# Kernel optimization log

Hardware: AMD Instinct MI355X
Metric: run time of the kernel (lower is better)

## Reference

```python
import jax, jax.numpy as jnp
import numpy as np

B, L, D_MODEL = 4, 2048, 1024
N_HEADS, FEAT, HEAD_DIM = 16, 16, 64
CHUNK = 128
EPS = 1e-12


def taylor_exp(x):
    """2nd-order Taylor feature map of exp(q.k/sqrt(d)).
    x: (b, h, l, f) -> (b, h, l, 1 + f + f*f)"""
    f = x.shape[-1]
    r2 = jnp.sqrt(jnp.asarray(2.0, x.dtype))
    rd = jnp.sqrt(jnp.asarray(float(f), x.dtype))      # sqrt(d)
    rrd = jnp.sqrt(rd)                                  # d**0.25
    x2 = (x[..., :, None] * x[..., None, :]).reshape(*x.shape[:-1], f * f) / r2
    ones = jnp.ones_like(x[..., :1])
    return jnp.concatenate([ones, x / rrd, x2 / rd], axis=-1)


def setup_inputs() -> dict:
    key = jax.random.key(0)
    k1, k2, k3, k4, k5 = jax.random.split(key, 5)
    s = 0.02
    return {
        "hidden_states": jax.random.normal(k1, (B, L, D_MODEL), jnp.float32),
        "Wq": jax.random.normal(k2, (N_HEADS * FEAT, D_MODEL), jnp.float32) * s,
        "Wk": jax.random.normal(k3, (N_HEADS * FEAT, D_MODEL), jnp.float32) * s,
        "Wv": jax.random.normal(k4, (N_HEADS * HEAD_DIM, D_MODEL), jnp.float32) * s,
        "Wo": jax.random.normal(k5, (D_MODEL, N_HEADS * HEAD_DIM), jnp.float32) * s,
    }


def reference(hidden_states, Wq, Wk, Wv, Wo):
    b, l, _ = hidden_states.shape
    # projections (Linear without bias: x @ W.T)
    q = (hidden_states @ Wq.T).reshape(b, l, N_HEADS, FEAT).transpose(0, 2, 1, 3)
    k = (hidden_states @ Wk.T).reshape(b, l, N_HEADS, FEAT).transpose(0, 2, 1, 3)
    v = (hidden_states @ Wv.T).reshape(b, l, N_HEADS, HEAD_DIM).transpose(0, 2, 1, 3)

    qf = taylor_exp(q)  # (b, h, l, De) with De = 1 + f + f^2 = 273
    kf = taylor_exp(k)
    De = qf.shape[-1]

    # chunked causal linear attention: same math as cumulative kv-state
    n = l // CHUNK
    qc = jnp.moveaxis(qf.reshape(b, N_HEADS, n, CHUNK, De), 2, 0)       # (n,b,h,c,De)
    kc = jnp.moveaxis(kf.reshape(b, N_HEADS, n, CHUNK, De), 2, 0)
    vc = jnp.moveaxis(v.reshape(b, N_HEADS, n, CHUNK, HEAD_DIM), 2, 0)
    mask = jnp.tril(jnp.ones((CHUNK, CHUNK), qf.dtype))

    def step(carry, xs):
        S, z = carry                       # S: (b,h,De,e), z: (b,h,De)
        qi, ki, vi = xs
        attn = jnp.einsum('bhid,bhjd->bhij', qi, ki) * mask
        num = jnp.einsum('bhij,bhje->bhie', attn, vi) \
            + jnp.einsum('bhid,bhde->bhie', qi, S)
        den = attn.sum(-1) + jnp.einsum('bhid,bhd->bhi', qi, z)
        yi = num / (den[..., None] + EPS)
        S = S + jnp.einsum('bhjd,bhje->bhde', ki, vi)
        z = z + ki.sum(2)
        return (S, z), yi

    S0 = jnp.zeros((b, N_HEADS, De, HEAD_DIM), qf.dtype)
    z0 = jnp.zeros((b, N_HEADS, De), qf.dtype)
    _, ys = jax.lax.scan(step, (S0, z0), (qc, kc, vc))
    y = jnp.moveaxis(ys, 0, 2).reshape(b, N_HEADS, l, HEAD_DIM)          # (b,h,l,e)
    y = y.transpose(0, 2, 1, 3).reshape(b, l, N_HEADS * HEAD_DIM)        # (b,l,h*e)
    return y @ Wo.T
```

## Files before the change

kernel.cpp:

```cpp
#include <hip/hip_runtime.h>
#include <hip/hip_bf16.h>

#define BB 4
#define LL 2048
#define DM 1024
#define NH 16
#define FEAT 16
#define HD 64
#define CHUNK 128
#define NCHUNK 16
#define NEXT 80
#define SROW 23040
#define EPS 1e-12f
#define INV_R2RD 0.17677669529663688f
#define QKVLD 1536

typedef short bf16x8_t __attribute__((ext_vector_type(8)));
typedef float f32x4_t  __attribute__((ext_vector_type(4)));

__device__ __forceinline__ float b2f(unsigned short u) {
    union { unsigned int i; float f; } x; x.i = ((unsigned int)u) << 16; return x.f;
}
__device__ __forceinline__ unsigned short f2b(float f) {
    __hip_bfloat16 h = __float2bfloat16(f);
    return *reinterpret_cast<unsigned short*>(&h);
}

__global__ __launch_bounds__(256)
void cast_all(const float* __restrict__ hs, const float* __restrict__ wq,
              const float* __restrict__ wk, const float* __restrict__ wv,
              const float* __restrict__ wo, unsigned short* __restrict__ hs_bf,
              unsigned short* __restrict__ wqkv, unsigned short* __restrict__ wo_bf)
{
    const int i = (blockIdx.x * 256 + threadIdx.x) * 4;
    const float* s; unsigned short* d;
    if (i < 8388608)       { s = hs + i;             d = hs_bf + i; }
    else if (i < 8650752)  { s = wq + (i - 8388608); d = wqkv + (i - 8388608); }
    else if (i < 8912896)  { s = wk + (i - 8650752); d = wqkv + 262144 + (i - 8650752); }
    else if (i < 9961472)  { s = wv + (i - 8912896); d = wqkv + 524288 + (i - 8912896); }
    else if (i < 11010048) { s = wo + (i - 9961472); d = wo_bf + (i - 9961472); }
    else return;
    float4 v = *(const float4*)s;
    ushort4 o; o.x = f2b(v.x); o.y = f2b(v.y); o.z = f2b(v.z); o.w = f2b(v.w);
    *(ushort4*)d = o;
}

template <typename OutT>
__global__ __launch_bounds__(512, 2)
void gemm_bf16_8ph(const unsigned short* __restrict__ A, const unsigned short* __restrict__ Bw,
                   OutT* __restrict__ C, int K, int lda, int ldb, int ldc)
{
    __shared__ unsigned short lds[65536];
    const int tid  = threadIdx.x;
    const int wid  = tid >> 6, lane = tid & 63;
    const int wm   = wid >> 2, wn = wid & 3;
    const int ml   = lane & 15, quad = lane >> 4;
    const int nwg = gridDim.x * gridDim.y;
    const int lin = blockIdx.y * gridDim.x + blockIdx.x;
    const int swz_id = (lin & 7) * (nwg >> 3) + (lin >> 3);
    const int m0   = (swz_id / gridDim.x) * 256, n0 = (swz_id % gridDim.x) * 256;
    const int NT   = K >> 6;

    const int srow  = tid >> 3;
    const int scol  = ((tid & 7) ^ (srow & 7)) << 3;
    const int wbase = wid << 9;

    auto stage_half = [&](int t, int isB, int h) {
        const unsigned short* g0 = isB ? Bw : A;
        const int ld = isB ? ldb : lda;
        const int rb = (isB ? n0 : m0) + h * 128 + srow;
        const int k0 = t << 6;
        unsigned short* lb = lds + (isB ? 32768 : 0) + ((t & 1) << 14) + (h << 13) + wbase;
#pragma unroll
        for (int l = 0; l < 2; ++l) {
            const unsigned short* g = g0 + (size_t)(rb + l * 64) * ld + k0 + scol;
            __builtin_amdgcn_global_load_lds((const __attribute__((address_space(1))) void*)g,
                                             (__attribute__((address_space(3))) void*)(lb + l * 4096),
                                             16, 0, 0);
        }
    };

    f32x4_t acc[8][4];
#pragma unroll
    for (int i = 0; i < 8; ++i)
#pragma unroll
        for (int j = 0; j < 4; ++j) acc[i][j] = (f32x4_t){0.f, 0.f, 0.f, 0.f};

    stage_half(0, 0, 0); stage_half(0, 1, 0); stage_half(0, 0, 1); stage_half(0, 1, 1);
    stage_half(1, 0, 0); stage_half(1, 1, 0); stage_half(1, 0, 1);
    asm volatile("s_waitcnt vmcnt(6)" ::: "memory");
    __builtin_amdgcn_s_barrier();

    const int swz  = (ml & 7) << 3;
    const int c0   = (quad << 3) ^ swz;
    const int c1   = (32 + (quad << 3)) ^ swz;
    const int arow = ml << 6;

    bf16x8_t aA[4][2], bLo[2][2], bHi[2][2];

    for (int t = 0; t < NT; ++t) {
        const int ab = (t & 1) << 14;
        const int bb = 32768 + ((t & 1) << 14);

#pragma unroll
        for (int m = 0; m < 4; ++m) {
            const int r = ab + ((2 * m + wm) << 10) + arow;
            aA[m][0] = *(const bf16x8_t*)&lds[r + c0];
            aA[m][1] = *(const bf16x8_t*)&lds[r + c1];
        }
#pragma unroll
        for (int n = 0; n < 2; ++n) {
            const int r = bb + ((4 * n + wn) << 10) + arow;
            bLo[n][0] = *(const bf16x8_t*)&lds[r + c0];
            bLo[n][1] = *(const bf16x8_t*)&lds[r + c1];
        }
        if (t + 1 < NT) stage_half(t + 1, 1, 1);
        __builtin_amdgcn_s_barrier();
        asm volatile("s_waitcnt lgkmcnt(0)" ::: "memory");
        __builtin_amdgcn_sched_barrier(0);
        __builtin_amdgcn_s_setprio(1);
#pragma unroll
        for (int m = 0; m < 4; ++m)
#pragma unroll
            for (int n = 0; n < 2; ++n) {
                acc[m][n] = __builtin_amdgcn_mfma_f32_16x16x32_bf16(aA[m][0], bLo[n][0], acc[m][n], 0, 0, 0);
                acc[m][n] = __builtin_amdgcn_mfma_f32_16x16x32_bf16(aA[m][1], bLo[n][1], acc[m][n], 0, 0, 0);
            }
        __builtin_amdgcn_s_setprio(0);
        __builtin_amdgcn_s_barrier();

#pragma unroll
        for (int n = 0; n < 2; ++n) {
            const int r = bb + ((4 * (n + 2) + wn) << 10) + arow;
            bHi[n][0] = *(const bf16x8_t*)&lds[r + c0];
            bHi[n][1] = *(const bf16x8_t*)&lds[r + c1];
        }
        if (t + 2 < NT) stage_half(t + 2, 0, 0);
        __builtin_amdgcn_s_barrier();
        asm volatile("s_waitcnt lgkmcnt(0)" ::: "memory");
        __builtin_amdgcn_sched_barrier(0);
        __builtin_amdgcn_s_setprio(1);
#pragma unroll
        for (int m = 0; m < 4; ++m)
#pragma unroll
            for (int n = 0; n < 2; ++n) {
                acc[m][2 + n] = __builtin_amdgcn_mfma_f32_16x16x32_bf16(aA[m][0], bHi[n][0], acc[m][2 + n], 0, 0, 0);
                acc[m][2 + n] = __builtin_amdgcn_mfma_f32_16x16x32_bf16(aA[m][1], bHi[n][1], acc[m][2 + n], 0, 0, 0);
            }
        __builtin_amdgcn_s_setprio(0);
        __builtin_amdgcn_s_barrier();

#pragma unroll
        for (int m = 0; m < 4; ++m) {
            const int r = ab + ((2 * (m + 4) + wm) << 10) + arow;
            aA[m][0] = *(const bf16x8_t*)&lds[r + c0];
            aA[m][1] = *(const bf16x8_t*)&lds[r + c1];
        }
        if (t + 2 < NT) stage_half(t + 2, 1, 0);
        __builtin_amdgcn_s_barrier();
        asm volatile("s_waitcnt lgkmcnt(0)" ::: "memory");
        __builtin_amdgcn_sched_barrier(0);
        __builtin_amdgcn_s_setprio(1);
#pragma unroll
        for (int m = 0; m < 4; ++m)
#pragma unroll
            for (int n = 0; n < 2; ++n) {
                acc[4 + m][2 + n] = __builtin_amdgcn_mfma_f32_16x16x32_bf16(aA[m][0], bHi[n][0], acc[4 + m][2 + n], 0, 0, 0);
                acc[4 + m][2 + n] = __builtin_amdgcn_mfma_f32_16x16x32_bf16(aA[m][1], bHi[n][1], acc[4 + m][2 + n], 0, 0, 0);
            }
        __builtin_amdgcn_s_setprio(0);
        __builtin_amdgcn_s_barrier();

        if (t + 2 < NT) stage_half(t + 2, 0, 1);
        __builtin_amdgcn_s_barrier();
        asm volatile("s_waitcnt lgkmcnt(0)" ::: "memory");
        __builtin_amdgcn_sched_barrier(0);
        __builtin_amdgcn_s_setprio(1);
#pragma unroll
        for (int m = 0; m < 4; ++m)
#pragma unroll
            for (int n = 0; n < 2; ++n) {
                acc[4 + m][n] = __builtin_amdgcn_mfma_f32_16x16x32_bf16(aA[m][0], bLo[n][0], acc[4 + m][n], 0, 0, 0);
                acc[4 + m][n] = __builtin_amdgcn_mfma_f32_16x16x32_bf16(aA[m][1], bLo[n][1], acc[4 + m][n], 0, 0, 0);
            }
        __builtin_amdgcn_s_setprio(0);
        if (t + 2 < NT)      asm volatile("s_waitcnt vmcnt(6)" ::: "memory");
        else if (t + 1 < NT) asm volatile("s_waitcnt vmcnt(0)" ::: "memory");
        __builtin_amdgcn_s_barrier();
    }

#pragma unroll
    for (int m = 0; m < 8; ++m) {
        const int rbase = m0 + (2 * m + wm) * 16 + quad * 4;
#pragma unroll
        for (int n = 0; n < 4; ++n) {
            const int col = n0 + (4 * n + wn) * 16 + ml;
#pragma unroll
            for (int r = 0; r < 4; ++r) {
                const float v = acc[m][n][r];
                if constexpr (sizeof(OutT) == 2) {
                    ((unsigned short*)C)[(size_t)(rbase + r) * ldc + col] = f2b(v);
                } else {
                    ((float*)C)[(size_t)(rbase + r) * ldc + col] = v;
                }
            }
        }
    }
}

__global__ __launch_bounds__(512, 2)
void gemm_bf16_128x256(const unsigned short* __restrict__ A, const unsigned short* __restrict__ Bw,
                       float* __restrict__ C, int K, int lda, int ldb, int ldc)
{
    __shared__ unsigned short lds[49152];
    const int tid  = threadIdx.x;
    const int wid  = tid >> 6, lane = tid & 63;
    const int wm   = wid >> 2, wn = wid & 3;
    const int ml   = lane & 15, quad = lane >> 4;
    const int nwg = gridDim.x * gridDim.y;
    const int lin = blockIdx.y * gridDim.x + blockIdx.x;
    const int swz_id = (lin & 7) * (nwg >> 3) + (lin >> 3);
    const int m0   = (swz_id / gridDim.x) * 128, n0 = (swz_id % gridDim.x) * 256;
    const int NT   = K >> 6;

    const int srow  = tid >> 3;
    const int scol  = ((tid & 7) ^ (srow & 7)) << 3;
    const int wbase = wid << 9;

    auto stage_unit = [&](int t, int isB, int u) {
        const unsigned short* g0 = isB ? Bw : A;
        const int ld = isB ? ldb : lda;
        const int rb = (isB ? n0 : m0) + u * 64 + srow;
        const int k0 = t << 6;
        unsigned short* lb = lds + (isB ? 16384 : 0) + ((t & 1) << (isB ? 14 : 13))
                             + (u << 12) + wbase;
        const unsigned short* g = g0 + (size_t)rb * ld + k0 + scol;
        __builtin_amdgcn_global_load_lds((const __attribute__((address_space(1))) void*)g,
                                         (__attribute__((address_space(3))) void*)lb, 16, 0, 0);
    };

    f32x4_t acc[4][4];
#pragma unroll
    for (int i = 0; i < 4; ++i)
#pragma unroll
        for (int j = 0; j < 4; ++j) acc[i][j] = (f32x4_t){0.f, 0.f, 0.f, 0.f};

    stage_unit(0, 0, 0); stage_unit(0, 0, 1);
    stage_unit(0, 1, 0); stage_unit(0, 1, 1); stage_unit(0, 1, 2); stage_unit(0, 1, 3);
    stage_unit(1, 0, 0); stage_unit(1, 0, 1);
    stage_unit(1, 1, 0); stage_unit(1, 1, 1);
    asm volatile("s_waitcnt vmcnt(4)" ::: "memory");
    __builtin_amdgcn_s_barrier();

    const int swz  = (ml & 7) << 3;
    const int c0   = (quad << 3) ^ swz;
    const int c1   = (32 + (quad << 3)) ^ swz;
    const int arow = ml << 6;

    bf16x8_t aA[4][2], bF[2][2];

    for (int t = 0; t < NT; ++t) {
        const int ab = (t & 1) << 13;
        const int bb = 16384 + ((t & 1) << 14);

#pragma unroll
        for (int m = 0; m < 4; ++m) {
            const int r = ab + ((2 * m + wm) << 10) + arow;
            aA[m][0] = *(const bf16x8_t*)&lds[r + c0];
            aA[m][1] = *(const bf16x8_t*)&lds[r + c1];
        }
#pragma unroll
        for (int n = 0; n < 2; ++n) {
            const int r = bb + ((4 * n + wn) << 10) + arow;
            bF[n][0] = *(const bf16x8_t*)&lds[r + c0];
            bF[n][1] = *(const bf16x8_t*)&lds[r + c1];
        }
        if (t + 1 < NT) { stage_unit(t + 1, 1, 2); stage_unit(t + 1, 1, 3); }
        __builtin_amdgcn_s_barrier();
        asm volatile("s_waitcnt lgkmcnt(0)" ::: "memory");
        __builtin_amdgcn_sched_barrier(0);
        __builtin_amdgcn_s_setprio(1);
#pragma unroll
        for (int m = 0; m < 4; ++m)
#pragma unroll
            for (int n = 0; n < 2; ++n) {
                acc[m][n] = __builtin_amdgcn_mfma_f32_16x16x32_bf16(aA[m][0], bF[n][0], acc[m][n], 0, 0, 0);
                acc[m][n] = __builtin_amdgcn_mfma_f32_16x16x32_bf16(aA[m][1], bF[n][1], acc[m][n], 0, 0, 0);
            }
        __builtin_amdgcn_s_setprio(0);
        __builtin_amdgcn_s_barrier();

#pragma unroll
        for (int n = 0; n < 2; ++n) {
            const int r = bb + ((4 * (n + 2) + wn) << 10) + arow;
            bF[n][0] = *(const bf16x8_t*)&lds[r + c0];
            bF[n][1] = *(const bf16x8_t*)&lds[r + c1];
        }
        if (t + 2 < NT) {
            stage_unit(t + 2, 0, 0); stage_unit(t + 2, 0, 1);
            stage_unit(t + 2, 1, 0); stage_unit(t + 2, 1, 1);
        }
        __builtin_amdgcn_s_barrier();
        asm volatile("s_waitcnt lgkmcnt(0)" ::: "memory");
        __builtin_amdgcn_sched_barrier(0);
        __builtin_amdgcn_s_setprio(1);
#pragma unroll
        for (int m = 0; m < 4; ++m)
#pragma unroll
            for (int n = 0; n < 2; ++n) {
                acc[m][2 + n] = __builtin_amdgcn_mfma_f32_16x16x32_bf16(aA[m][0], bF[n][0], acc[m][2 + n], 0, 0, 0);
                acc[m][2 + n] = __builtin_amdgcn_mfma_f32_16x16x32_bf16(aA[m][1], bF[n][1], acc[m][2 + n], 0, 0, 0);
            }
        __builtin_amdgcn_s_setprio(0);
        if (t + 2 < NT)      asm volatile("s_waitcnt vmcnt(4)" ::: "memory");
        else if (t + 1 < NT) asm volatile("s_waitcnt vmcnt(0)" ::: "memory");
        __builtin_amdgcn_s_barrier();
    }

#pragma unroll
    for (int m = 0; m < 4; ++m) {
        const int rbase = m0 + (2 * m + wm) * 16 + quad * 4;
#pragma unroll
        for (int n = 0; n < 4; ++n) {
            const int col = n0 + (4 * n + wn) * 16 + ml;
#pragma unroll
            for (int r = 0; r < 4; ++r)
                C[(size_t)(rbase + r) * ldc + col] = acc[m][n][r];
        }
    }
}

__global__ __launch_bounds__(256)
void state_kernel(const unsigned short* __restrict__ qkv, unsigned short* __restrict__ STg)
{
    __shared__ unsigned short KT[16 * 136];
    __shared__ unsigned short VT[80 * 136];

    const int x = blockIdx.x;
    const int c = x & 15, bh = x >> 4;
    const int b = bh >> 4, h = bh & 15;
    const int tid = threadIdx.x;
    const int wave = tid >> 6, lane = tid & 63;
    const int ml = lane & 15, kg8 = (lane >> 4) * 8;
    const size_t rowbase = (size_t)(b * LL + c * CHUNK);
    const size_t Sbase = (size_t)x * SROW;

    {
        const int row = tid >> 1, half = tid & 1;
        uint4 kv = *(const uint4*)(qkv + (rowbase + row) * QKVLD + 256 + h * 16 + half * 8);
        const unsigned short* kp = (const unsigned short*)&kv;
#pragma unroll
        for (int i = 0; i < 8; ++i) KT[(half * 8 + i) * 136 + row] = kp[i];
#pragma unroll
        for (int cc = 0; cc < 4; ++cc) {
            uint4 vv = *(const uint4*)(qkv + (rowbase + row) * QKVLD + 512 + h * 64 + half * 32 + cc * 8);
            const unsigned short* vp = (const unsigned short*)&vv;
#pragma unroll
            for (int i = 0; i < 8; ++i) VT[(half * 32 + cc * 8 + i) * 136 + row] = vp[i];
        }
        if (half == 0) {
            VT[64 * 136 + row] = 0x3F80;
        } else {
#pragma unroll
            for (int e = 65; e < 80; ++e) VT[e * 136 + row] = 0;
        }
    }
    __syncthreads();

    bf16x8_t bfr[5][4];
#pragma unroll
    for (int nt = 0; nt < 5; ++nt)
#pragma unroll
        for (int ks = 0; ks < 4; ++ks)
            bfr[nt][ks] = *(const bf16x8_t*)&VT[(nt * 16 + ml) * 136 + ks * 32 + kg8];

    for (int mt = wave; mt < 18; mt += 4) {
        const int d = mt * 16 + ml;
        bf16x8_t af[4];
#pragma unroll
        for (int ks = 0; ks < 4; ++ks) {
            const int jb = ks * 32 + kg8;
            unsigned short o[8];
            if (d >= 24 && d < 280) {
                const int e = d - 24, a = e >> 4, bq = e & 15;
                bf16x8_t ka = *(const bf16x8_t*)&KT[a  * 136 + jb];
                bf16x8_t kb = *(const bf16x8_t*)&KT[bq * 136 + jb];
#pragma unroll
                for (int j = 0; j < 8; ++j)
                    o[j] = f2b(b2f((unsigned short)ka[j]) * b2f((unsigned short)kb[j]) * INV_R2RD);
            } else if (d == 0) {
#pragma unroll
                for (int j = 0; j < 8; ++j) o[j] = 0x3F80;
            } else if (d <= 16) {
                bf16x8_t kx = *(const bf16x8_t*)&KT[(d - 1) * 136 + jb];
#pragma unroll
                for (int j = 0; j < 8; ++j) o[j] = f2b(b2f((unsigned short)kx[j]) * 0.5f);
            } else {
#pragma unroll
                for (int j = 0; j < 8; ++j) o[j] = 0;
            }
            af[ks] = *(const bf16x8_t*)o;
        }
        f32x4_t acc[5];
#pragma unroll
        for (int nt = 0; nt < 5; ++nt) acc[nt] = (f32x4_t){0.f, 0.f, 0.f, 0.f};
        __builtin_amdgcn_s_setprio(1);
#pragma unroll
        for (int nt = 0; nt < 5; ++nt)
#pragma unroll
            for (int ks = 0; ks < 4; ++ks)
                acc[nt] = __builtin_amdgcn_mfma_f32_16x16x32_bf16(af[ks], bfr[nt][ks], acc[nt], 0, 0, 0);
        __builtin_amdgcn_s_setprio(0);
#pragma unroll
        for (int nt = 0; nt < 5; ++nt) {
            ushort4 pk;
            pk.x = f2b(acc[nt][0]); pk.y = f2b(acc[nt][1]);
            pk.z = f2b(acc[nt][2]); pk.w = f2b(acc[nt][3]);
            *(ushort4*)(STg + Sbase + (size_t)mt * 1280 + (nt * 16 + ml) * 16 + (lane >> 4) * 4) = pk;
        }
    }
}

__global__ __launch_bounds__(256)
void scan_S(unsigned short* __restrict__ STg) {
    const int bh  = blockIdx.y;
    const int idx = blockIdx.x * 256 + threadIdx.x;
    if (idx >= SROW / 8) return;
    const size_t base = (size_t)bh * NCHUNK * SROW + (size_t)idx * 8;
    uint4 v[NCHUNK];
#pragma unroll
    for (int c = 0; c < NCHUNK; ++c)
        v[c] = *(const uint4*)(STg + base + (size_t)c * SROW);
    float acc[8] = {};
#pragma unroll
    for (int c = 0; c < NCHUNK; ++c) {
        const unsigned short* vp = (const unsigned short*)&v[c];
        uint4 o;
        unsigned short* op = (unsigned short*)&o;
#pragma unroll
        for (int i = 0; i < 8; ++i) { op[i] = f2b(acc[i]); acc[i] += b2f(vp[i]); }
        *(uint4*)(STg + base + (size_t)c * SROW) = o;
    }
}

#define OFF_VT 0
#define OFF_QP 0
#define OFF_KP 5120
#define OFF_A  10880
#define OFF_QS 28288

__global__ __launch_bounds__(256)
void out_kernel(const unsigned short* __restrict__ qkv_ro, const unsigned short* __restrict__ STg,
                unsigned short* __restrict__ qkv_w)
{
    __shared__ unsigned short smem[30336];

    const int x = blockIdx.x;
    const int c = x & 15, bh = x >> 4;
    const int b = bh >> 4, h = bh & 15;
    const int tid = threadIdx.x;
    const int w = tid >> 6, lane = tid & 63;
    const int ml = lane & 15, quad = lane >> 4, kg8 = quad * 8;
    const size_t rowbase = (size_t)(b * LL + c * CHUNK);
    const size_t Sbase = (size_t)x * SROW;

    const unsigned short* stp = STg + Sbase + (size_t)(quad >> 1) * 1280 + (quad & 1) * 8;
    bf16x8_t stf[2][5];
#pragma unroll
    for (int nt = 0; nt < 5; ++nt)
        stf[0][nt] = *(const bf16x8_t*)(stp + (nt * 16 + ml) * 16);

    {
        const int row = tid >> 1, half = tid & 1;
        uint4 qv = *(const uint4*)(qkv_ro + (rowbase + row) * QKVLD + h * 16 + half * 8);
        *(uint4*)&smem[OFF_QP + row * 40 + half * 8] = qv;
        *(uint4*)&smem[OFF_QP + row * 40 + 16 + half * 8] = (uint4){0, 0, 0, 0};
        *(uint4*)&smem[OFF_QS + row * 16 + half * 8] = qv;
        uint4 kv = *(const uint4*)(qkv_ro + (rowbase + row) * QKVLD + 256 + h * 16 + half * 8);
        *(uint4*)&smem[OFF_KP + row * 40 + half * 8] = kv;
        *(uint4*)&smem[OFF_KP + row * 40 + 16 + half * 8] = (uint4){0, 0, 0, 0};
    }
    __syncthreads();

    {
        bf16x8_t q0 = *(const bf16x8_t*)&smem[OFF_QP + (w * 32 + ml) * 40 + kg8];
        bf16x8_t q1 = *(const bf16x8_t*)&smem[OFF_QP + (w * 32 + 16 + ml) * 40 + kg8];
#pragma unroll
        for (int nt = 0; nt < 8; ++nt) {
            bf16x8_t kf = *(const bf16x8_t*)&smem[OFF_KP + (nt * 16 + ml) * 40 + kg8];
            f32x4_t a0 = __builtin_amdgcn_mfma_f32_16x16x32_bf16(q0, kf, (f32x4_t){0,0,0,0}, 0, 0, 0);
            f32x4_t a1 = __builtin_amdgcn_mfma_f32_16x16x32_bf16(q1, kf, (f32x4_t){0,0,0,0}, 0, 0, 0);
            const int j = nt * 16 + ml;
#pragma unroll
            for (int r = 0; r < 4; ++r) {
                int i0 = w * 32 + quad * 4 + r;
                float s0 = a0[r] * 0.25f;
                float v0 = (j <= i0) ? (1.f + s0 + 0.5f * s0 * s0) : 0.f;
                smem[OFF_A + i0 * 136 + j] = f2b(v0);
                int i1 = i0 + 16;
                float s1 = a1[r] * 0.25f;
                float v1 = (j <= i1) ? (1.f + s1 + 0.5f * s1 * s1) : 0.f;
                smem[OFF_A + i1 * 136 + j] = f2b(v1);
            }
        }
    }
    const int r0 = w * 32 + ml, r1 = r0 + 16;
    float qA[16], qB[16];
    {
        bf16x8_t t0 = *(const bf16x8_t*)&smem[OFF_QS + r0 * 16];
        bf16x8_t t1 = *(const bf16x8_t*)&smem[OFF_QS + r0 * 16 + 8];
        bf16x8_t t2 = *(const bf16x8_t*)&smem[OFF_QS + r1 * 16];
        bf16x8_t t3 = *(const bf16x8_t*)&smem[OFF_QS + r1 * 16 + 8];
#pragma unroll
        for (int i = 0; i < 8; ++i) {
            qA[i] = b2f((unsigned short)t0[i]); qA[8 + i] = b2f((unsigned short)t1[i]);
            qB[i] = b2f((unsigned short)t2[i]); qB[8 + i] = b2f((unsigned short)t3[i]);
        }
    }
    __syncthreads();

    {
        const int row = tid >> 1, half = tid & 1;
#pragma unroll
        for (int cc = 0; cc < 4; ++cc) {
            uint4 vv = *(const uint4*)(qkv_ro + (rowbase + row) * QKVLD + 512 + h * 64 + half * 32 + cc * 8);
            const unsigned short* vp = (const unsigned short*)&vv;
#pragma unroll
            for (int i = 0; i < 8; ++i) smem[OFF_VT + (half * 32 + cc * 8 + i) * 136 + row] = vp[i];
        }
        if (half == 0) {
            smem[OFF_VT + 64 * 136 + row] = 0x3F80;
        } else {
#pragma unroll
            for (int e = 65; e < 80; ++e) smem[OFF_VT + e * 136 + row] = 0;
        }
    }
    __syncthreads();

    f32x4_t acc[2][5];
#pragma unroll
    for (int mt = 0; mt < 2; ++mt)
#pragma unroll
        for (int nt = 0; nt < 5; ++nt) acc[mt][nt] = (f32x4_t){0.f, 0.f, 0.f, 0.f};

#pragma unroll
    for (int ks = 0; ks < 4; ++ks) {
        bf16x8_t af0 = *(const bf16x8_t*)&smem[OFF_A + (w * 32 + ml) * 136 + ks * 32 + kg8];
        bf16x8_t af1 = *(const bf16x8_t*)&smem[OFF_A + (w * 32 + 16 + ml) * 136 + ks * 32 + kg8];
        __builtin_amdgcn_s_setprio(1);
#pragma unroll
        for (int nt = 0; nt < 5; ++nt) {
            bf16x8_t bv = *(const bf16x8_t*)&smem[OFF_VT + (nt * 16 + ml) * 136 + ks * 32 + kg8];
            acc[0][nt] = __builtin_amdgcn_mfma_f32_16x16x32_bf16(af0, bv, acc[0][nt], 0, 0, 0);
            acc[1][nt] = __builtin_amdgcn_mfma_f32_16x16x32_bf16(af1, bv, acc[1][nt], 0, 0, 0);
        }
        __builtin_amdgcn_s_setprio(0);
    }

#pragma unroll
    for (int kq = 0; kq < 9; ++kq) {
        if (kq < 8) {
#pragma unroll
            for (int nt = 0; nt < 5; ++nt)
                stf[(kq + 1) & 1][nt] =
                    *(const bf16x8_t*)(stp + (size_t)(kq + 1) * 2560 + (nt * 16 + ml) * 16);
        }
        bf16x8_t qf[2];
#pragma unroll
        for (int mt = 0; mt < 2; ++mt) {
            const float* q = (mt == 0) ? qA : qB;
            const int qsrow = (mt == 0) ? r0 : r1;
            const int d0 = kq * 32 + kg8;
            unsigned short o[8];
            if (d0 >= 24 && d0 < 280) {
                const int e0 = d0 - 24;
                const float qa = b2f(smem[OFF_QS + qsrow * 16 + (e0 >> 4)]) * INV_R2RD;
                if ((e0 & 15) == 0) {
#pragma unroll
                    for (int j = 0; j < 8; ++j) o[j] = f2b(qa * q[j]);
                } else {
#pragma unroll
                    for (int j = 0; j < 8; ++j) o[j] = f2b(qa * q[8 + j]);
                }
            } else if (d0 == 0) {
                o[0] = 0x3F80;
#pragma unroll
                for (int j = 1; j < 8; ++j) o[j] = f2b(q[j - 1] * 0.5f);
            } else if (d0 == 8) {
#pragma unroll
                for (int j = 0; j < 8; ++j) o[j] = f2b(q[7 + j] * 0.5f);
            } else if (d0 == 16) {
                o[0] = f2b(q[15] * 0.5f);
#pragma unroll
                for (int j = 1; j < 8; ++j) o[j] = 0;
            } else {
#pragma unroll
                for (int j = 0; j < 8; ++j) o[j] = 0;
            }
            qf[mt] = *(const bf16x8_t*)o;
        }
        __builtin_amdgcn_s_setprio(1);
#pragma unroll
        for (int nt = 0; nt < 5; ++nt) {
            acc[0][nt] = __builtin_amdgcn_mfma_f32_16x16x32_bf16(qf[0], stf[kq & 1][nt], acc[0][nt], 0, 0, 0);
            acc[1][nt] = __builtin_amdgcn_mfma_f32_16x16x32_bf16(qf[1], stf[kq & 1][nt], acc[1][nt], 0, 0, 0);
        }
        __builtin_amdgcn_s_setprio(0);
    }

#pragma unroll
    for (int mt = 0; mt < 2; ++mt) {
        float den[4];
#pragma unroll
        for (int r = 0; r < 4; ++r) den[r] = __shfl(acc[mt][4][r], lane & 48);
#pragma unroll
        for (int r = 0; r < 4; ++r) {
            const size_t grow = rowbase + w * 32 + mt * 16 + quad * 4 + r;
            const float rc = 1.f / (den[r] + EPS);
#pragma unroll
            for (int nt = 0; nt < 4; ++nt)
                qkv_w[grow * QKVLD + 512 + h * 64 + nt * 16 + ml] = f2b(acc[mt][nt][r] * rc);
        }
    }
}

extern "C" void kernel_launch(void* const* d_in, const int* in_sizes, int n_in,
                              void* d_out, int out_size, void* d_ws, size_t ws_size,
                              hipStream_t stream)
{
    (void)in_sizes; (void)n_in; (void)out_size; (void)ws_size;
    const float* hs = (const float*)d_in[0];
    const float* Wq = (const float*)d_in[1];
    const float* Wk = (const float*)d_in[2];
    const float* Wv = (const float*)d_in[3];
    const float* Wo = (const float*)d_in[4];
    float* out = (float*)d_out;

    char* ws = (char*)d_ws;
    unsigned short* STg   = (unsigned short*)ws;
    unsigned short* hs_bf = (unsigned short*)ws;
    size_t off = 47185920;
    unsigned short* qkv   = (unsigned short*)(ws + off); off += 25165824;
    unsigned short* Wqkv  = (unsigned short*)(ws + off); off += 3145728;
    unsigned short* Wo_bf = (unsigned short*)(ws + off); off += 2097152;

    cast_all<<<10752, 256, 0, stream>>>(hs, Wq, Wk, Wv, Wo, hs_bf, Wqkv, Wo_bf);
    gemm_bf16_8ph<unsigned short><<<dim3(6, 32), 512, 0, stream>>>(hs_bf, Wqkv, qkv,
                                                                   DM, DM, DM, QKVLD);
    state_kernel<<<1024, 256, 0, stream>>>(qkv, STg);
    scan_S<<<dim3(12, 64), 256, 0, stream>>>(STg);
    out_kernel<<<1024, 256, 0, stream>>>(qkv, STg, qkv);
    gemm_bf16_128x256<<<dim3(4, 64), 512, 0, stream>>>(qkv + 512, Wo_bf, out,
                                                       DM, QKVLD, DM, DM);
}
```

Before: 201.9 us.

## Compact per-chunk state layout and triple-buffer state loads in output kernel

```diff
diff --git a/kernel.cpp b/kernel.cpp
--- a/kernel.cpp
+++ b/kernel.cpp
@@ -9,8 +9,8 @@
 #define HD 64
 #define CHUNK 128
 #define NCHUNK 16
-#define NEXT 80
-#define SROW 23040
+#define NEXT 65
+#define SROW 18720
 #define EPS 1e-12f
 #define INV_R2RD 0.17677669529663688f
 #define QKVLD 1536
@@ -342,6 +342,7 @@
     const int tid = threadIdx.x;
     const int wave = tid >> 6, lane = tid & 63;
     const int ml = lane & 15, kg8 = (lane >> 4) * 8;
+    const int quad4 = (lane >> 4) * 4;
     const size_t rowbase = (size_t)(b * LL + c * CHUNK);
     const size_t Sbase = (size_t)x * SROW;
 
@@ -416,7 +417,11 @@
             ushort4 pk;
             pk.x = f2b(acc[nt][0]); pk.y = f2b(acc[nt][1]);
             pk.z = f2b(acc[nt][2]); pk.w = f2b(acc[nt][3]);
-            *(ushort4*)(STg + Sbase + (size_t)mt * 1280 + (nt * 16 + ml) * 16 + (lane >> 4) * 4) = pk;
+            if (nt < 4) {
+                *(ushort4*)(STg + Sbase + (size_t)mt * 1040 + (nt * 16 + ml) * 16 + quad4) = pk;
+            } else if (ml == 0) {
+                *(ushort4*)(STg + Sbase + (size_t)mt * 1040 + 1024 + quad4) = pk;
+            }
         }
     }
 }
@@ -447,13 +452,12 @@
 #define OFF_QP 0
 #define OFF_KP 5120
 #define OFF_A  10880
-#define OFF_QS 28288
 
 __global__ __launch_bounds__(256)
 void out_kernel(const unsigned short* __restrict__ qkv_ro, const unsigned short* __restrict__ STg,
                 unsigned short* __restrict__ qkv_w)
 {
-    __shared__ unsigned short smem[30336];
+    __shared__ unsigned short smem[28288];
 
     const int x = blockIdx.x;
     const int c = x & 15, bh = x >> 4;
@@ -464,22 +468,28 @@
     const size_t rowbase = (size_t)(b * LL + c * CHUNK);
     const size_t Sbase = (size_t)x * SROW;
 
-    const unsigned short* stp = STg + Sbase + (size_t)(quad >> 1) * 1280 + (quad & 1) * 8;
-    bf16x8_t stf[2][5];
-#pragma unroll
-    for (int nt = 0; nt < 5; ++nt)
-        stf[0][nt] = *(const bf16x8_t*)(stp + (nt * 16 + ml) * 16);
-
-    {
-        const int row = tid >> 1, half = tid & 1;
-        uint4 qv = *(const uint4*)(qkv_ro + (rowbase + row) * QKVLD + h * 16 + half * 8);
-        *(uint4*)&smem[OFF_QP + row * 40 + half * 8] = qv;
-        *(uint4*)&smem[OFF_QP + row * 40 + 16 + half * 8] = (uint4){0, 0, 0, 0};
-        *(uint4*)&smem[OFF_QS + row * 16 + half * 8] = qv;
-        uint4 kv = *(const uint4*)(qkv_ro + (rowbase + row) * QKVLD + 256 + h * 16 + half * 8);
-        *(uint4*)&smem[OFF_KP + row * 40 + half * 8] = kv;
-        *(uint4*)&smem[OFF_KP + row * 40 + 16 + half * 8] = (uint4){0, 0, 0, 0};
-    }
+    const unsigned short* stp = STg + Sbase + (size_t)(quad >> 1) * 1040 + (quad & 1) * 8;
+    bf16x8_t stf[3][5];
+    auto ldst = [&](int kq, int slot) {
+#pragma unroll
+        for (int nt = 0; nt < 5; ++nt)
+            stf[slot][nt] = *(const bf16x8_t*)(stp + (size_t)kq * 2080 + (nt * 16 + ml) * 16);
+    };
+
+    const int row = tid >> 1, half = tid & 1;
+    uint4 qv = *(const uint4*)(qkv_ro + (rowbase + row) * QKVLD + h * 16 + half * 8);
+    uint4 kv = *(const uint4*)(qkv_ro + (rowbase + row) * QKVLD + 256 + h * 16 + half * 8);
+    uint4 vreg[4];
+#pragma unroll
+    for (int cc = 0; cc < 4; ++cc)
+        vreg[cc] = *(const uint4*)(qkv_ro + (rowbase + row) * QKVLD + 512 + h * 64 + half * 32 + cc * 8);
+    ldst(0, 0);
+    ldst(1, 1);
+
+    *(uint4*)&smem[OFF_QP + row * 40 + half * 8] = qv;
+    *(uint4*)&smem[OFF_QP + row * 40 + 16 + half * 8] = (uint4){0, 0, 0, 0};
+    *(uint4*)&smem[OFF_KP + row * 40 + half * 8] = kv;
+    *(uint4*)&smem[OFF_KP + row * 40 + 16 + half * 8] = (uint4){0, 0, 0, 0};
     __syncthreads();
 
     {
@@ -507,24 +517,28 @@
     const int r0 = w * 32 + ml, r1 = r0 + 16;
     float qA[16], qB[16];
     {
-        bf16x8_t t0 = *(const bf16x8_t*)&smem[OFF_QS + r0 * 16];
-        bf16x8_t t1 = *(const bf16x8_t*)&smem[OFF_QS + r0 * 16 + 8];
-        bf16x8_t t2 = *(const bf16x8_t*)&smem[OFF_QS + r1 * 16];
-        bf16x8_t t3 = *(const bf16x8_t*)&smem[OFF_QS + r1 * 16 + 8];
+        bf16x8_t t0 = *(const bf16x8_t*)&smem[OFF_QP + r0 * 40];
+        bf16x8_t t1 = *(const bf16x8_t*)&smem[OFF_QP + r0 * 40 + 8];
+        bf16x8_t t2 = *(const bf16x8_t*)&smem[OFF_QP + r1 * 40];
+        bf16x8_t t3 = *(const bf16x8_t*)&smem[OFF_QP + r1 * 40 + 8];
 #pragma unroll
         for (int i = 0; i < 8; ++i) {
             qA[i] = b2f((unsigned short)t0[i]); qA[8 + i] = b2f((unsigned short)t1[i]);
             qB[i] = b2f((unsigned short)t2[i]); qB[8 + i] = b2f((unsigned short)t3[i]);
         }
     }
+    float qselA[8], qselB[8];
+#pragma unroll
+    for (int j = 0; j < 8; ++j) {
+        qselA[j] = (quad & 1) ? qA[j] : qA[8 + j];
+        qselB[j] = (quad & 1) ? qB[j] : qB[8 + j];
+    }
     __syncthreads();
 
     {
-        const int row = tid >> 1, half = tid & 1;
 #pragma unroll
         for (int cc = 0; cc < 4; ++cc) {
-            uint4 vv = *(const uint4*)(qkv_ro + (rowbase + row) * QKVLD + 512 + h * 64 + half * 32 + cc * 8);
-            const unsigned short* vp = (const unsigned short*)&vv;
+            const unsigned short* vp = (const unsigned short*)&vreg[cc];
 #pragma unroll
             for (int i = 0; i < 8; ++i) smem[OFF_VT + (half * 32 + cc * 8 + i) * 136 + row] = vp[i];
         }
@@ -542,6 +556,8 @@
     for (int mt = 0; mt < 2; ++mt)
 #pragma unroll
         for (int nt = 0; nt < 5; ++nt) acc[mt][nt] = (f32x4_t){0.f, 0.f, 0.f, 0.f};
+
+    ldst(2, 2);
 
 #pragma unroll
     for (int ks = 0; ks < 4; ++ks) {
@@ -559,29 +575,21 @@
 
 #pragma unroll
     for (int kq = 0; kq < 9; ++kq) {
-        if (kq < 8) {
-#pragma unroll
-            for (int nt = 0; nt < 5; ++nt)
-                stf[(kq + 1) & 1][nt] =
-                    *(const bf16x8_t*)(stp + (size_t)(kq + 1) * 2560 + (nt * 16 + ml) * 16);
-        }
         bf16x8_t qf[2];
 #pragma unroll
         for (int mt = 0; mt < 2; ++mt) {
-            const float* q = (mt == 0) ? qA : qB;
-            const int qsrow = (mt == 0) ? r0 : r1;
+            const float* q    = (mt == 0) ? qA : qB;
+            const float* qsel = (mt == 0) ? qselA : qselB;
             const int d0 = kq * 32 + kg8;
             unsigned short o[8];
             if (d0 >= 24 && d0 < 280) {
-                const int e0 = d0 - 24;
-                const float qa = b2f(smem[OFF_QS + qsrow * 16 + (e0 >> 4)]) * INV_R2RD;
-                if ((e0 & 15) == 0) {
-#pragma unroll
-                    for (int j = 0; j < 8; ++j) o[j] = f2b(qa * q[j]);
-                } else {
-#pragma unroll
-                    for (int j = 0; j < 8; ++j) o[j] = f2b(qa * q[8 + j]);
-                }
+                const int i2 = 2 * kq;
+                const float base = (quad == 3) ? q[i2 > 15 ? 15 : i2]
+                                 : (quad == 0) ? q[i2 < 2 ? 0 : i2 - 2]
+                                               : q[i2 < 1 ? 0 : i2 - 1];
+                const float qa = base * INV_R2RD;
+#pragma unroll
+                for (int j = 0; j < 8; ++j) o[j] = f2b(qa * qsel[j]);
             } else if (d0 == 0) {
                 o[0] = 0x3F80;
 #pragma unroll
@@ -602,10 +610,11 @@
         __builtin_amdgcn_s_setprio(1);
 #pragma unroll
         for (int nt = 0; nt < 5; ++nt) {
-            acc[0][nt] = __builtin_amdgcn_mfma_f32_16x16x32_bf16(qf[0], stf[kq & 1][nt], acc[0][nt], 0, 0, 0);
-            acc[1][nt] = __builtin_amdgcn_mfma_f32_16x16x32_bf16(qf[1], stf[kq & 1][nt], acc[1][nt], 0, 0, 0);
-        }
-        __builtin_amdgcn_s_setprio(0);
+            acc[0][nt] = __builtin_amdgcn_mfma_f32_16x16x32_bf16(qf[0], stf[kq % 3][nt], acc[0][nt], 0, 0, 0);
+            acc[1][nt] = __builtin_amdgcn_mfma_f32_16x16x32_bf16(qf[1], stf[kq % 3][nt], acc[1][nt], 0, 0, 0);
+        }
+        __builtin_amdgcn_s_setprio(0);
+        if (kq + 3 < 9) ldst(kq + 3, kq % 3);
     }
 
 #pragma unroll
@@ -648,7 +657,7 @@
     gemm_bf16_8ph<unsigned short><<<dim3(6, 32), 512, 0, stream>>>(hs_bf, Wqkv, qkv,
                                                                    DM, DM, DM, QKVLD);
     state_kernel<<<1024, 256, 0, stream>>>(qkv, STg);
-    scan_S<<<dim3(12, 64), 256, 0, stream>>>(STg);
+    scan_S<<<dim3(10, 64), 256, 0, stream>>>(STg);
     out_kernel<<<1024, 256, 0, stream>>>(qkv, STg, qkv);
     gemm_bf16_128x256<<<dim3(4, 64), 512, 0, stream>>>(qkv + 512, Wo_bf, out,
                                                        DM, QKVLD, DM, DM);
```

New measurement: 198.3 us. Within noise of the previous version (-1.8%).
